# Kernel optimization log

Measured on AMD Instinct MI355X. Metric: run time of the kernel, lower is better.

## Reference

```python
import jax, jax.numpy as jnp
import numpy as np

D_MODEL = 1024
NUM_HEADS = 16
HEAD_DIM = D_MODEL // NUM_HEADS
B, T = 2, 2048


def setup_inputs() -> dict:
    key = jax.random.key(0)
    kx, kq, kk, kv, ko = jax.random.split(key, 5)
    s = 1.0 / np.sqrt(D_MODEL)  # ~Linear init scale
    return {
        "x": jax.random.normal(kx, (B, T, D_MODEL), dtype=jnp.float32),
        "Wq": jax.random.normal(kq, (D_MODEL, D_MODEL), dtype=jnp.float32) * s,
        "Wk": jax.random.normal(kk, (D_MODEL, D_MODEL), dtype=jnp.float32) * s,
        "Wv": jax.random.normal(kv, (D_MODEL, D_MODEL), dtype=jnp.float32) * s,
        "Wo": jax.random.normal(ko, (D_MODEL, D_MODEL), dtype=jnp.float32) * s,
    }


def reference(x, Wq, Wk, Wv, Wo):
    Bc, Tc, _ = x.shape
    H, D = NUM_HEADS, HEAD_DIM
    scale = jnp.sqrt(jnp.asarray(D, x.dtype))
    # torch Linear (bias=False): y = x @ W^T
    q = (x @ Wq.T).reshape(Bc, Tc, H, D).transpose(0, 2, 1, 3)  # [B,H,T,D]
    k = (x @ Wk.T).reshape(Bc, Tc, H, D).transpose(0, 2, 1, 3)
    v = (x @ Wv.T).reshape(Bc, Tc, H, D).transpose(0, 2, 1, 3)
    scores = jnp.einsum("bhtd,bhsd->bhts", q, k) / scale  # [B,H,T,T]
    # causal bias: upper triangle (strictly future positions) gets -1e9
    causal_bias = jnp.triu(jnp.ones((Tc, Tc), dtype=jnp.float32), k=1) * -1e9
    scores = scores + causal_bias
    weights = jax.nn.softmax(scores, axis=-1)
    # dropout is identity in eval / p=0
    out = jnp.einsum("bhts,bhsd->bhtd", weights, v)  # [B,H,T,D]
    out = out.transpose(0, 2, 1, 3).reshape(Bc, Tc, H * D)
    return out @ Wo.T
```

## Files before the change

### kernel.cpp

```cpp
#include <hip/hip_runtime.h>
#include <hip/hip_bf16.h>

typedef __bf16 bf16_t;
typedef __bf16 bf16x2 __attribute__((ext_vector_type(2)));
typedef __bf16 bf16x4 __attribute__((ext_vector_type(4)));
typedef __bf16 bf16x8 __attribute__((ext_vector_type(8)));
typedef float  f32x4  __attribute__((ext_vector_type(4)));
typedef int    i32x2  __attribute__((ext_vector_type(2)));

#define D_MODEL 1024
#define HEADS   16
#define HD      64
#define BB      2
#define TT      2048
#define MROWS   (BB*TT)

#define GLDS16(g, l) __builtin_amdgcn_global_load_lds( \
    (const __attribute__((address_space(1))) void*)(g), \
    (__attribute__((address_space(3))) void*)(l), 16, 0, 0)

static __device__ __forceinline__ int pack_bf16(float a, float b) {
    bf16x2 t; t[0] = (bf16_t)a; t[1] = (bf16_t)b;
    return __builtin_bit_cast(int, t);
}

__global__ __launch_bounds__(256) void cvt_all_kernel(const float* __restrict__ x,
                                                      const float* __restrict__ wq,
                                                      const float* __restrict__ wk,
                                                      const float* __restrict__ wv,
                                                      const float* __restrict__ wo,
                                                      bf16_t* __restrict__ dst) {
    const int i = blockIdx.x * 256 + threadIdx.x;
    const float* src;
    int s;
    if (i < 1048576) { src = x; s = i; }
    else {
        int j = i - 1048576;
        int w = j >> 18;
        s = j & 262143;
        src = (w == 0) ? wq : (w == 1) ? wk : (w == 2) ? wv : wo;
    }
    float4 v = reinterpret_cast<const float4*>(src)[s];
    bf16x4 o;
    o[0] = (bf16_t)v.x; o[1] = (bf16_t)v.y; o[2] = (bf16_t)v.z; o[3] = (bf16_t)v.w;
    reinterpret_cast<bf16x4*>(dst)[i] = o;
}

template<int MODE, int BN>
__global__ __launch_bounds__(256, 3) void gemm_bt(const bf16_t* __restrict__ A,
                                                  const bf16_t* __restrict__ Bw,
                                                  void* __restrict__ Cout,
                                                  int M, int N, int K) {
    constexpr int NI = BN / 32;
    __shared__ __align__(16) bf16_t As[128*64];
    __shared__ __align__(16) bf16_t Bs[BN*64];
    const int tid   = threadIdx.x;
    const int lane  = tid & 63;
    const int wave  = tid >> 6;
    const int col16 = lane & 15;
    const int quad  = lane >> 4;
    const int wrow  = (wave & 1) * 64;
    const int wcol  = (wave >> 1) * (BN / 2);
    const int bm    = blockIdx.y * 128;
    const int bn    = blockIdx.x * BN;
    const int x7    = col16 & 7;

    const int lr = tid >> 3;
    const int lc = ((tid & 7) ^ (lr & 7)) * 8;

    const bf16_t* agp = &A [(size_t)(bm + lr)*K + lc];
    const bf16_t* bgp = &Bw[(size_t)(bn + lr)*K + lc];

    f32x4 acc[4][NI];
#pragma unroll
    for (int i = 0; i < 4; i++)
#pragma unroll
        for (int j = 0; j < NI; j++) acc[i][j] = (f32x4){0.f, 0.f, 0.f, 0.f};

    for (int k0 = 0; k0 < K; k0 += 64) {
#pragma unroll
        for (int s = 0; s < 4; s++)
            GLDS16(agp + k0 + (size_t)s*32*K, &As[s*2048 + wave*512]);
#pragma unroll
        for (int s = 0; s < BN/32; s++)
            GLDS16(bgp + k0 + (size_t)s*32*K, &Bs[s*2048 + wave*512]);
        __syncthreads();

        bf16x8 af[4][2], bfr[NI][2];
#pragma unroll
        for (int mi = 0; mi < 4; mi++)
#pragma unroll
            for (int h = 0; h < 2; h++)
                af[mi][h] = *reinterpret_cast<const bf16x8*>(
                    &As[(wrow + mi*16 + col16)*64 + ((h*4 + quad) ^ x7)*8]);
#pragma unroll
        for (int ni = 0; ni < NI; ni++)
#pragma unroll
            for (int h = 0; h < 2; h++)
                bfr[ni][h] = *reinterpret_cast<const bf16x8*>(
                    &Bs[(wcol + ni*16 + col16)*64 + ((h*4 + quad) ^ x7)*8]);
#pragma unroll
        for (int mi = 0; mi < 4; mi++)
#pragma unroll
            for (int ni = 0; ni < NI; ni++) {
                acc[mi][ni] = __builtin_amdgcn_mfma_f32_16x16x32_bf16(af[mi][0], bfr[ni][0], acc[mi][ni], 0, 0, 0);
                acc[mi][ni] = __builtin_amdgcn_mfma_f32_16x16x32_bf16(af[mi][1], bfr[ni][1], acc[mi][ni], 0, 0, 0);
            }
        __syncthreads();
    }

#pragma unroll
    for (int mi = 0; mi < 4; mi++) {
        const int gm = bm + wrow + mi*16 + quad*4;
        const int t  = gm & (TT - 1);
        const int b  = gm >> 11;
#pragma unroll
        for (int ni = 0; ni < NI; ni++) {
            const int gn = bn + wcol + ni*16 + col16;
            if (MODE == 2) {
#pragma unroll
                for (int r = 0; r < 4; r++)
                    reinterpret_cast<float*>(Cout)[(size_t)(gm + r) * N + gn] = acc[mi][ni][r];
            } else {
                const int which = gn >> 10;
                const int n = gn & 1023;
                const int h = n >> 6, d = n & 63;
                if (which == 2) {
                    bf16x4 o4;
#pragma unroll
                    for (int r = 0; r < 4; r++) o4[r] = (bf16_t)acc[mi][ni][r];
                    bf16_t* vt = reinterpret_cast<bf16_t*>(Cout) + (size_t)2 * MROWS * D_MODEL;
                    *reinterpret_cast<bf16x4*>(&vt[(((size_t)(b*HEADS + h))*HD + d)*TT + t]) = o4;
                } else {
                    bf16_t* base = reinterpret_cast<bf16_t*>(Cout) + (size_t)which * MROWS * D_MODEL;
#pragma unroll
                    for (int r = 0; r < 4; r++) {
                        float v = acc[mi][ni][r];
                        if (which == 0) v *= 0.18033688f;
                        base[(((size_t)(b*HEADS + h))*TT + (t + r))*HD + d] = (bf16_t)v;
                    }
                }
            }
        }
    }
}

__global__ __launch_bounds__(256, 4) void attn_kernel(const bf16_t* __restrict__ Q,
                                                      const bf16_t* __restrict__ Kk,
                                                      const bf16_t* __restrict__ Vt,
                                                      bf16_t* __restrict__ O) {
    __shared__ __align__(16) bf16_t Ks[2][64*64];
    __shared__ __align__(16) bf16_t Vs[2][64*64];

    const int tid   = threadIdx.x;
    const int lane  = tid & 63;
    const int wave  = tid >> 6;
    const int col16 = lane & 15;
    const int quad  = lane >> 4;
    const int kw    = wave & 1;
    const int qw    = wave >> 1;

    const int bx = blockIdx.x;
    const int r_ = bx >> 8, s_ = bx & 255;
    const int bh = s_ & 31;
    const int g  = s_ >> 5;
    const int qt = (r_ == 0) ? (31 - g)
                 : (r_ == 1) ? g
                 : (r_ == 2) ? (15 - g)
                             : (16 + g);
    const int qb    = qt * 64;
    const int qbase = qb + qw * 32;
    const int nkt   = qt + 1;

    const bf16_t* Qb = Q  + (size_t)bh * TT * HD;
    const bf16_t* Kb = Kk + (size_t)bh * TT * HD;
    const bf16_t* Vb = Vt + (size_t)bh * HD * TT;

    bf16x8 qf[2][2];
#pragma unroll
    for (int qg = 0; qg < 2; qg++)
#pragma unroll
        for (int h = 0; h < 2; h++)
            qf[qg][h] = *reinterpret_cast<const bf16x8*>(
                &Qb[(size_t)(qbase + qg*16 + col16)*HD + h*32 + quad*8]);

    const int srow = (tid >> 3) & 31;
    const int sg   = ((lane & 7) ^ (srow & 7)) * 8;

    auto stage = [&](int kt, int buf) {
        const int s0 = kt * 64;
        GLDS16(&Kb[(size_t)(s0 + srow)*HD + sg],        &Ks[buf][wave*512]);
        GLDS16(&Kb[(size_t)(s0 + srow + 32)*HD + sg],   &Ks[buf][2048 + wave*512]);
        GLDS16(&Vb[(size_t)srow*TT + s0 + sg],          &Vs[buf][wave*512]);
        GLDS16(&Vb[(size_t)(srow + 32)*TT + s0 + sg],   &Vs[buf][2048 + wave*512]);
    };

    f32x4 acc[4][2];
#pragma unroll
    for (int i = 0; i < 4; i++)
#pragma unroll
        for (int j = 0; j < 2; j++) acc[i][j] = (f32x4){0.f,0.f,0.f,0.f};
    float lsum[2] = {0.f, 0.f};

    const int x7 = col16 & 7;

    stage(0, 0);
    __syncthreads();

    for (int kt = 0; kt < nkt; kt++) {
        const int buf = kt & 1;
        if (kt + 1 < nkt) stage(kt + 1, buf ^ 1);
        const int s0 = kt * 64;
        const bool diag = (kt == nkt - 1);

        bf16x8 kf0[2], kf1[2];
#pragma unroll
        for (int c = 0; c < 2; c++) {
            kf0[c] = *reinterpret_cast<const bf16x8*>(
                &Ks[buf][(kw*32 + c*16 + col16)*64 + ((0*4 + quad) ^ x7)*8]);
            kf1[c] = *reinterpret_cast<const bf16x8*>(
                &Ks[buf][(kw*32 + c*16 + col16)*64 + ((1*4 + quad) ^ x7)*8]);
        }

        int pk[2][2][2];
#pragma unroll
        for (int c = 0; c < 2; c++) {
#pragma unroll
            for (int qg = 0; qg < 2; qg++) {
                __builtin_amdgcn_s_setprio(1);
                f32x4 sv = __builtin_amdgcn_mfma_f32_16x16x32_bf16(kf0[c], qf[qg][0], (f32x4){0.f,0.f,0.f,0.f}, 0, 0, 0);
                sv       = __builtin_amdgcn_mfma_f32_16x16x32_bf16(kf1[c], qf[qg][1], sv, 0, 0, 0);
                __builtin_amdgcn_s_setprio(0);

                float pr[4];
#pragma unroll
                for (int r = 0; r < 4; r++) pr[r] = exp2f(sv[r]);
                if (diag) {
#pragma unroll
                    for (int r = 0; r < 4; r++)
                        if (s0 + kw*32 + c*16 + quad*4 + r > qbase + qg*16 + col16) pr[r] = 0.f;
                }
                lsum[qg] += (pr[0] + pr[1]) + (pr[2] + pr[3]);
                pk[c][qg][0] = pack_bf16(pr[0], pr[1]);
                pk[c][qg][1] = pack_bf16(pr[2], pr[3]);
            }
        }

        bf16x8 pf[2];
#pragma unroll
        for (int qg = 0; qg < 2; qg++) {
#if __has_builtin(__builtin_amdgcn_permlane32_swap)
            i32x2 u0 = __builtin_amdgcn_permlane32_swap(pk[0][qg][0], pk[1][qg][0], false, false);
            i32x2 v0 = __builtin_amdgcn_permlane16_swap(u0[0], u0[1], false, false);
            i32x2 u1 = __builtin_amdgcn_permlane32_swap(pk[0][qg][1], pk[1][qg][1], false, false);
            i32x2 v1 = __builtin_amdgcn_permlane16_swap(u1[0], u1[1], false, false);
            int4 bi = { v0[0], v1[0], v0[1], v1[1] };
#else
            const int a1 = ((quad & 1) * 32 + col16) * 4;
            const int a2 = a1 + 64;
            const bool hi = quad >= 2;
            int b0l = __builtin_amdgcn_ds_bpermute(a1, pk[0][qg][0]);
            int b0h = __builtin_amdgcn_ds_bpermute(a1, pk[1][qg][0]);
            int b1l = __builtin_amdgcn_ds_bpermute(a1, pk[0][qg][1]);
            int b1h = __builtin_amdgcn_ds_bpermute(a1, pk[1][qg][1]);
            int b2l = __builtin_amdgcn_ds_bpermute(a2, pk[0][qg][0]);
            int b2h = __builtin_amdgcn_ds_bpermute(a2, pk[1][qg][0]);
            int b3l = __builtin_amdgcn_ds_bpermute(a2, pk[0][qg][1]);
            int b3h = __builtin_amdgcn_ds_bpermute(a2, pk[1][qg][1]);
            int4 bi = { hi ? b0h : b0l, hi ? b1h : b1l, hi ? b2h : b2l, hi ? b3h : b3l };
#endif
            pf[qg] = __builtin_bit_cast(bf16x8, bi);
        }
        __builtin_amdgcn_s_setprio(1);
#pragma unroll
        for (int c = 0; c < 4; c++) {
            bf16x8 vf = *reinterpret_cast<const bf16x8*>(
                &Vs[buf][(c*16 + col16)*64 + ((kw*4 + quad) ^ x7)*8]);
            acc[c][0] = __builtin_amdgcn_mfma_f32_16x16x32_bf16(vf, pf[0], acc[c][0], 0, 0, 0);
            acc[c][1] = __builtin_amdgcn_mfma_f32_16x16x32_bf16(vf, pf[1], acc[c][1], 0, 0, 0);
        }
        __builtin_amdgcn_s_setprio(0);
        __syncthreads();
    }

#pragma unroll
    for (int qg = 0; qg < 2; qg++) {
        lsum[qg] += __shfl_xor(lsum[qg], 16);
        lsum[qg] += __shfl_xor(lsum[qg], 32);
    }

    float* Mq = qw ? reinterpret_cast<float*>(&Vs[0][0])
                   : reinterpret_cast<float*>(&Ks[0][0]);
    float* LS = reinterpret_cast<float*>(&Vs[0][0]) + 32*68;

    if (kw == 1) {
#pragma unroll
        for (int c = 0; c < 4; c++)
#pragma unroll
            for (int qg = 0; qg < 2; qg++)
                *reinterpret_cast<f32x4*>(&Mq[(qg*16 + col16)*68 + c*16 + quad*4]) = acc[c][qg];
        if (lane < 16) {
            LS[qw*32 + lane]      = lsum[0];
            LS[qw*32 + 16 + lane] = lsum[1];
        }
    }
    __syncthreads();

    if (kw == 0) {
        const int b_ = bh >> 4, h = bh & 15;
#pragma unroll
        for (int qg = 0; qg < 2; qg++) {
            const float l   = lsum[qg] + LS[qw*32 + qg*16 + col16];
            const float inv = 1.0f / l;
            const int t = qbase + qg*16 + col16;
            bf16_t* Ob = &O[(((size_t)(b_*TT + t))*HEADS + h)*HD + quad*4];
#pragma unroll
            for (int c = 0; c < 4; c++) {
                f32x4 m = *reinterpret_cast<const f32x4*>(&Mq[(qg*16 + col16)*68 + c*16 + quad*4]);
                bf16x4 o4;
#pragma unroll
                for (int r = 0; r < 4; r++) o4[r] = (bf16_t)((acc[c][qg][r] + m[r]) * inv);
                *reinterpret_cast<bf16x4*>(&Ob[c*16]) = o4;
            }
        }
    }
}

extern "C" void kernel_launch(void* const* d_in, const int* in_sizes, int n_in,
                              void* d_out, int out_size, void* d_ws, size_t ws_size,
                              hipStream_t stream) {
    const float* x  = (const float*)d_in[0];
    const float* Wq = (const float*)d_in[1];
    const float* Wk = (const float*)d_in[2];
    const float* Wv = (const float*)d_in[3];
    const float* Wo = (const float*)d_in[4];
    float* out = (float*)d_out;

    bf16_t* Xb  = (bf16_t*)d_ws;
    bf16_t* Wqb = Xb  + (size_t)MROWS * D_MODEL;
    bf16_t* Wob = Wqb + (size_t)3 * D_MODEL * D_MODEL;
    bf16_t* Qw  = Wob + (size_t)D_MODEL * D_MODEL;
    bf16_t* Kw  = Qw  + (size_t)MROWS * D_MODEL;
    bf16_t* Vt  = Kw  + (size_t)MROWS * D_MODEL;
    bf16_t* Ow  = Vt  + (size_t)MROWS * D_MODEL;

    cvt_all_kernel<<<(MROWS*D_MODEL + 4*D_MODEL*D_MODEL) / 4 / 256, 256, 0, stream>>>(
        x, Wq, Wk, Wv, Wo, Xb);

    dim3 gqkv(3 * D_MODEL / 128, MROWS / 128);
    gemm_bt<0,128><<<gqkv, 256, 0, stream>>>(Xb, Wqb, Qw, MROWS, 3 * D_MODEL, D_MODEL);

    attn_kernel<<<dim3(1024), 256, 0, stream>>>(Qw, Kw, Vt, Ow);

    dim3 go(D_MODEL / 64, MROWS / 128);
    gemm_bt<2,64><<<go, 256, 0, stream>>>(Ow, Wob, out, MROWS, D_MODEL, D_MODEL);
}
```

Before: 165.4 us.

## Process 128 query rows per attention block with 8 waves sharing KV tiles

The attention kernel moves from 256-thread blocks with 64-row query tiles to 512-thread blocks with 128-row query tiles, so four query-wave pairs share each staged K/V tile and the number of blocks is halved. Each thread now issues one staging load per tile instead of two. Waves whose query rows lie entirely before a key tile skip its compute but still hit the barrier, and the diagonal test is generalized per wave. The change adds dedicated shared memory for the cross-wave merge, which raises LDS use and can reduce occupancy. Some waves also sit idle on the last causal tile.

```diff
diff --git a/kernel.cpp b/kernel.cpp
--- a/kernel.cpp
+++ b/kernel.cpp
@@ -145,12 +145,14 @@
     }
 }
 
-__global__ __launch_bounds__(256, 4) void attn_kernel(const bf16_t* __restrict__ Q,
+__global__ __launch_bounds__(512, 4) void attn_kernel(const bf16_t* __restrict__ Q,
                                                       const bf16_t* __restrict__ Kk,
                                                       const bf16_t* __restrict__ Vt,
                                                       bf16_t* __restrict__ O) {
     __shared__ __align__(16) bf16_t Ks[2][64*64];
     __shared__ __align__(16) bf16_t Vs[2][64*64];
+    __shared__ __align__(16) float  Mm[4][32*68];
+    __shared__ float LSa[128];
 
     const int tid   = threadIdx.x;
     const int lane  = tid & 63;
@@ -164,13 +166,10 @@
     const int r_ = bx >> 8, s_ = bx & 255;
     const int bh = s_ & 31;
     const int g  = s_ >> 5;
-    const int qt = (r_ == 0) ? (31 - g)
-                 : (r_ == 1) ? g
-                 : (r_ == 2) ? (15 - g)
-                             : (16 + g);
-    const int qb    = qt * 64;
+    const int b  = (r_ == 0) ? (15 - g) : g;
+    const int qb    = b * 128;
     const int qbase = qb + qw * 32;
-    const int nkt   = qt + 1;
+    const int nkt   = 2 * b + 2;
 
     const bf16_t* Qb = Q  + (size_t)bh * TT * HD;
     const bf16_t* Kb = Kk + (size_t)bh * TT * HD;
@@ -184,15 +183,13 @@
             qf[qg][h] = *reinterpret_cast<const bf16x8*>(
                 &Qb[(size_t)(qbase + qg*16 + col16)*HD + h*32 + quad*8]);
 
-    const int srow = (tid >> 3) & 31;
+    const int srow = tid >> 3;
     const int sg   = ((lane & 7) ^ (srow & 7)) * 8;
 
     auto stage = [&](int kt, int buf) {
         const int s0 = kt * 64;
-        GLDS16(&Kb[(size_t)(s0 + srow)*HD + sg],        &Ks[buf][wave*512]);
-        GLDS16(&Kb[(size_t)(s0 + srow + 32)*HD + sg],   &Ks[buf][2048 + wave*512]);
-        GLDS16(&Vb[(size_t)srow*TT + s0 + sg],          &Vs[buf][wave*512]);
-        GLDS16(&Vb[(size_t)(srow + 32)*TT + s0 + sg],   &Vs[buf][2048 + wave*512]);
+        GLDS16(&Kb[(size_t)(s0 + srow)*HD + sg], &Ks[buf][wave*512]);
+        GLDS16(&Vb[(size_t)srow*TT + s0 + sg],   &Vs[buf][wave*512]);
     };
 
     f32x4 acc[4][2];
@@ -211,7 +208,9 @@
         const int buf = kt & 1;
         if (kt + 1 < nkt) stage(kt + 1, buf ^ 1);
         const int s0 = kt * 64;
-        const bool diag = (kt == nkt - 1);
+
+        if (s0 <= qbase + 31) {
+        const bool diag = (s0 + 63 > qbase);
 
         bf16x8 kf0[2], kf1[2];
 #pragma unroll
@@ -280,6 +279,8 @@
             acc[c][1] = __builtin_amdgcn_mfma_f32_16x16x32_bf16(vf, pf[1], acc[c][1], 0, 0, 0);
         }
         __builtin_amdgcn_s_setprio(0);
+        }
+
         __syncthreads();
     }
 
@@ -289,19 +290,15 @@
         lsum[qg] += __shfl_xor(lsum[qg], 32);
     }
 
-    float* Mq = qw ? reinterpret_cast<float*>(&Vs[0][0])
-                   : reinterpret_cast<float*>(&Ks[0][0]);
-    float* LS = reinterpret_cast<float*>(&Vs[0][0]) + 32*68;
-
     if (kw == 1) {
 #pragma unroll
         for (int c = 0; c < 4; c++)
 #pragma unroll
             for (int qg = 0; qg < 2; qg++)
-                *reinterpret_cast<f32x4*>(&Mq[(qg*16 + col16)*68 + c*16 + quad*4]) = acc[c][qg];
+                *reinterpret_cast<f32x4*>(&Mm[qw][(qg*16 + col16)*68 + c*16 + quad*4]) = acc[c][qg];
         if (lane < 16) {
-            LS[qw*32 + lane]      = lsum[0];
-            LS[qw*32 + 16 + lane] = lsum[1];
+            LSa[qw*32 + lane]      = lsum[0];
+            LSa[qw*32 + 16 + lane] = lsum[1];
         }
     }
     __syncthreads();
@@ -310,13 +307,13 @@
         const int b_ = bh >> 4, h = bh & 15;
 #pragma unroll
         for (int qg = 0; qg < 2; qg++) {
-            const float l   = lsum[qg] + LS[qw*32 + qg*16 + col16];
+            const float l   = lsum[qg] + LSa[qw*32 + qg*16 + col16];
             const float inv = 1.0f / l;
             const int t = qbase + qg*16 + col16;
             bf16_t* Ob = &O[(((size_t)(b_*TT + t))*HEADS + h)*HD + quad*4];
 #pragma unroll
             for (int c = 0; c < 4; c++) {
-                f32x4 m = *reinterpret_cast<const f32x4*>(&Mq[(qg*16 + col16)*68 + c*16 + quad*4]);
+                f32x4 m = *reinterpret_cast<const f32x4*>(&Mm[qw][(qg*16 + col16)*68 + c*16 + quad*4]);
                 bf16x4 o4;
 #pragma unroll
                 for (int r = 0; r < 4; r++) o4[r] = (bf16_t)((acc[c][qg][r] + m[r]) * inv);
@@ -350,7 +347,7 @@
     dim3 gqkv(3 * D_MODEL / 128, MROWS / 128);
     gemm_bt<0,128><<<gqkv, 256, 0, stream>>>(Xb, Wqb, Qw, MROWS, 3 * D_MODEL, D_MODEL);
 
-    attn_kernel<<<dim3(1024), 256, 0, stream>>>(Qw, Kw, Vt, Ow);
+    attn_kernel<<<dim3(512), 512, 0, stream>>>(Qw, Kw, Vt, Ow);
 
     dim3 go(D_MODEL / 64, MROWS / 128);
     gemm_bt<2,64><<<go, 256, 0, stream>>>(Ow, Wob, out, MROWS, D_MODEL, D_MODEL);
```

Measured after the change: 183.3 us. 10.8% more time.
